# Performance work log

Hardware: AMD Instinct MI355X
Metric: run time of the kernel (lower is better)

The kernel has to match this reference:

```python
import jax, jax.numpy as jnp
import numpy as np

N_NODES = 50000
N_EDGES = 1600000
N_FEAT = 128
DROPOUT = 0.1


def setup_inputs() -> dict:
    key = jax.random.key(0)
    k1, k2, k3, k4 = jax.random.split(key, 4)
    x = jax.random.normal(k1, (N_NODES, N_FEAT), dtype=jnp.float32)
    adj_vals = jax.random.uniform(k2, (N_EDGES,), dtype=jnp.float32)
    row = jax.random.randint(k3, (N_EDGES,), 0, N_NODES, dtype=jnp.int32)
    col = jax.random.randint(k4, (N_EDGES,), 0, N_NODES, dtype=jnp.int32)
    return {"x": x, "adj_vals": adj_vals, "row": row, "col": col}


def reference(x, adj_vals, row, col):
    # MixedDropout on sparse adjacency values (deterministic fixed key),
    # then SpMM: out[i] = sum_{e: row[e]==i} A_drop[e] * x[col[e]]
    keep_prob = 1.0 - DROPOUT
    mask_key = jax.random.fold_in(jax.random.key(42), 7)
    keep = jax.random.bernoulli(mask_key, keep_prob, adj_vals.shape)
    vals_drop = jnp.where(keep, adj_vals / keep_prob, 0.0)
    # gather source features and weight by (dropped) edge values
    msgs = vals_drop[:, None] * x[col]  # [E, F]
    out = jax.ops.segment_sum(msgs, row, num_segments=N_NODES)  # [N, F]
    return out
```

## Files before the change

### kernel.cpp

```cpp
#include <hip/hip_runtime.h>
#include <stdint.h>

#define N_NODES 50000
#define N_EDGES 1600000
#define N_FEAT 128
#define CAP 64
#define OVF_CAP 65536

#define RSHIFT 8
#define BROWS 256
#define NB 196
#define NWG_A 250
#define A_THREADS 1024
#define CHUNKS_PW 1600
#define CAPW 56


struct KeyPair { uint32_t a, b; };

__host__ __device__ constexpr inline uint32_t rotl32(uint32_t x, int r) {
  return (x << r) | (x >> (32 - r));
}

__host__ __device__ constexpr inline KeyPair threefry2x32(uint32_t k0, uint32_t k1,
                                                          uint32_t x0, uint32_t x1) {
  const uint32_t ks0 = k0, ks1 = k1, ks2 = k0 ^ k1 ^ 0x1BD11BDAu;
  x0 += ks0;
  x1 += ks1;
  const int rotA[4] = {13, 15, 26, 6};
  const int rotB[4] = {17, 29, 16, 24};
  const uint32_t ks[3] = {ks0, ks1, ks2};
  for (int i = 0; i < 5; ++i) {
    const int* rot = (i & 1) ? rotB : rotA;
    for (int j = 0; j < 4; ++j) {
      x0 += x1;
      x1 = rotl32(x1, rot[j]);
      x1 ^= x0;
    }
    x0 += ks[(i + 1) % 3];
    x1 += ks[(i + 2) % 3] + (uint32_t)(i + 1);
  }
  return {x0, x1};
}

constexpr KeyPair MASK_KEY = threefry2x32(0u, 42u, 0u, 7u);

__device__ inline bool edge_keep(uint32_t e) {
  KeyPair r = threefry2x32(MASK_KEY.a, MASK_KEY.b, 0u, e);
  uint32_t bits = r.a ^ r.b;
  float u = __uint_as_float((bits >> 9) | 0x3f800000u) - 1.0f;
  return u < 0.9f;
}

__device__ inline uint32_t f2bf(uint32_t b) {
  return (b + 0x7fffu + ((b >> 16) & 1u)) >> 16;
}

typedef uint32_t u2v __attribute__((ext_vector_type(2)));
typedef float f4v __attribute__((ext_vector_type(4)));


__global__ void __launch_bounds__(A_THREADS) convA_kernel(const float* __restrict__ x,
                                                          uint32_t* __restrict__ xb,
                                                          const float* __restrict__ adj_vals,
                                                          const int* __restrict__ row,
                                                          const int* __restrict__ col,
                                                          uint64_t* __restrict__ coarse,
                                                          uint32_t* __restrict__ lens,
                                                          uint32_t* __restrict__ ovf_count,
                                                          uint64_t* __restrict__ ovf) {
  __shared__ uint32_t cnt[NB];
  int wg = blockIdx.x;
  int tid = threadIdx.x;
  if (tid < NB) cnt[tid] = 0;

  const int gthreads = NWG_A * A_THREADS;
  for (int i = wg * A_THREADS + tid; i < (N_NODES * N_FEAT) / 4; i += gthreads) {
    float4 f = ((const float4*)x)[i];
    u2v o;
    o.x = f2bf(__float_as_uint(f.x)) | (f2bf(__float_as_uint(f.y)) << 16);
    o.y = f2bf(__float_as_uint(f.z)) | (f2bf(__float_as_uint(f.w)) << 16);
    __builtin_nontemporal_store(o, (u2v*)xb + i);
  }
  __syncthreads();

  for (int ch = tid; ch < CHUNKS_PW; ch += A_THREADS) {
    const int g = wg * CHUNKS_PW + ch;
    const int4 r4 = ((const int4*)row)[g];
    const int4 c4 = ((const int4*)col)[g];
    const float4 a4 = ((const float4*)adj_vals)[g];
    const int rr[4] = {r4.x, r4.y, r4.z, r4.w};
    const int cc[4] = {c4.x, c4.y, c4.z, c4.w};
    const float aa[4] = {a4.x, a4.y, a4.z, a4.w};
#pragma unroll
    for (int k = 0; k < 4; ++k) {
      const uint32_t e = (uint32_t)(4 * g + k);
      if (!edge_keep(e)) continue;
      const uint32_t r = (uint32_t)rr[k];
      const uint32_t c = (uint32_t)cc[k];
      const float v = aa[k] / 0.9f;
      const uint32_t b = r >> RSHIFT;
      const uint32_t li = atomicAdd(&cnt[b], 1u);
      const uint64_t p = ((uint64_t)r << 48) | ((uint64_t)c << 32) | (uint64_t)__float_as_uint(v);
      if (li < CAPW) {
        __builtin_nontemporal_store(p, coarse + ((size_t)b * NWG_A + wg) * CAPW + li);
      } else {
        const uint32_t oi = atomicAdd(ovf_count, 1u);
        if (oi < OVF_CAP) ovf[oi] = p;
      }
    }
  }
  __syncthreads();
  if (tid < NB) lens[(size_t)tid * NWG_A + wg] = min(cnt[tid], (uint32_t)CAPW);
}

__global__ void __launch_bounds__(1024) partB_kernel(const uint64_t* __restrict__ coarse,
                                                     const uint32_t* __restrict__ lens,
                                                     uint32_t* __restrict__ payload,
                                                     uint32_t* __restrict__ cursor,
                                                     uint32_t* __restrict__ ovf_count,
                                                     uint64_t* __restrict__ ovf) {
  int b = blockIdx.x;
  int tid = threadIdx.x;
  __shared__ uint32_t cnt[BROWS];
  if (tid < BROWS) cnt[tid] = 0;
  __syncthreads();

  int wave = tid >> 6;
  int lane = tid & 63;
  for (int seg = wave; seg < NWG_A; seg += 16) {
    uint32_t len = lens[(size_t)b * NWG_A + seg];
    if (lane < (int)len) {
      uint64_t p = coarse[((size_t)b * NWG_A + seg) * CAPW + lane];
      uint32_t r = (uint32_t)(p >> 48);
      uint32_t rl = r & (BROWS - 1);
      uint32_t idx = atomicAdd(&cnt[rl], 1u);
      if (idx < CAP) {
        uint32_t c = (uint32_t)(p >> 32) & 0xFFFFu;
        payload[(size_t)r * CAP + idx] = (c << 16) | f2bf((uint32_t)p);
      } else {
        uint32_t oi = atomicAdd(ovf_count, 1u);
        if (oi < OVF_CAP) ovf[oi] = p;
      }
    }
  }
  __syncthreads();
  if (tid < BROWS) {
    uint32_t r = ((uint32_t)b << RSHIFT) + (uint32_t)tid;
    if (r < N_NODES) cursor[r] = min(cnt[tid], (uint32_t)CAP);
  }
}

__global__ void __launch_bounds__(256) gather_bf16_kernel(const uint32_t* __restrict__ xb,
                                                          const uint32_t* __restrict__ payload,
                                                          const uint32_t* __restrict__ cursor,
                                                          float* __restrict__ out) {
  int r = blockIdx.x * 16 + (threadIdx.x >> 4);
  int lane = threadIdx.x & 15;
  uint32_t base = (uint32_t)r * CAP;
  uint32_t cnt = cursor[r];
  if (cnt > CAP) cnt = CAP;
  const uint4* x4 = (const uint4*)xb;

  float acc0 = 0.f, acc1 = 0.f, acc2 = 0.f, acc3 = 0.f;
  float acc4 = 0.f, acc5 = 0.f, acc6 = 0.f, acc7 = 0.f;

  uint32_t p0 = __builtin_nontemporal_load(payload + base + lane);
  uint32_t p1 = (cnt > 16u) ? __builtin_nontemporal_load(payload + base + 16 + lane) : 0u;
  uint32_t p2 = (cnt > 32u) ? __builtin_nontemporal_load(payload + base + 32 + lane) : 0u;
  uint32_t p3 = (cnt > 48u) ? __builtin_nontemporal_load(payload + base + 48 + lane) : 0u;

#define GSTEP(ww)                                                            \
  {                                                                          \
    uint32_t cc = (ww) >> 16;                                                \
    float vv = __uint_as_float((ww) << 16);                                  \
    uint4 a = x4[(size_t)cc * 16 + lane];                                    \
    acc0 += vv * __uint_as_float(a.x << 16);                                 \
    acc1 += vv * __uint_as_float(a.x & 0xffff0000u);                         \
    acc2 += vv * __uint_as_float(a.y << 16);                                 \
    acc3 += vv * __uint_as_float(a.y & 0xffff0000u);                         \
    acc4 += vv * __uint_as_float(a.z << 16);                                 \
    acc5 += vv * __uint_as_float(a.z & 0xffff0000u);                         \
    acc6 += vv * __uint_as_float(a.w << 16);                                 \
    acc7 += vv * __uint_as_float(a.w & 0xffff0000u);                         \
  }

#define PCHUNK(preg, mm)                                                     \
  for (int j = 0; j < (mm); j += 8) {                                        \
    int lim = (mm) - j;                                                      \
    uint32_t w0 = __shfl((preg), j + 0, 16);                                 \
    uint32_t w1 = __shfl((preg), j + 1, 16);                                 \
    uint32_t w2 = __shfl((preg), j + 2, 16);                                 \
    uint32_t w3 = __shfl((preg), j + 3, 16);                                 \
    uint32_t w4 = __shfl((preg), j + 4, 16);                                 \
    uint32_t w5 = __shfl((preg), j + 5, 16);                                 \
    uint32_t w6 = __shfl((preg), j + 6, 16);                                 \
    uint32_t w7 = __shfl((preg), j + 7, 16);                                 \
    w1 = (1 < lim) ? w1 : 0u;                                                \
    w2 = (2 < lim) ? w2 : 0u;                                                \
    w3 = (3 < lim) ? w3 : 0u;                                                \
    w4 = (4 < lim) ? w4 : 0u;                                                \
    w5 = (5 < lim) ? w5 : 0u;                                                \
    w6 = (6 < lim) ? w6 : 0u;                                                \
    w7 = (7 < lim) ? w7 : 0u;                                                \
    GSTEP(w0) GSTEP(w1) GSTEP(w2) GSTEP(w3)                                  \
    GSTEP(w4) GSTEP(w5) GSTEP(w6) GSTEP(w7)                                  \
  }

  int rem = (int)cnt;
  if (rem > 0) {
    PCHUNK(p0, min(rem, 16));
    rem -= 16;
    if (rem > 0) {
      PCHUNK(p1, min(rem, 16));
      rem -= 16;
      if (rem > 0) {
        PCHUNK(p2, min(rem, 16));
        rem -= 16;
        if (rem > 0) {
          PCHUNK(p3, min(rem, 16));
        }
      }
    }
  }
#undef PCHUNK
#undef GSTEP

  f4v lo, hi;
  lo.x = acc0; lo.y = acc1; lo.z = acc2; lo.w = acc3;
  hi.x = acc4; hi.y = acc5; hi.z = acc6; hi.w = acc7;
  f4v* o = (f4v*)out + (size_t)r * 32 + lane * 2;
  __builtin_nontemporal_store(lo, o);
  __builtin_nontemporal_store(hi, o + 1);
}

__global__ void __launch_bounds__(256) ovf_pack_kernel(const float* __restrict__ x,
                                                       const uint32_t* __restrict__ ovf_count,
                                                       const uint64_t* __restrict__ ovf,
                                                       float* __restrict__ out) {
  uint32_t n = *ovf_count;
  if (n > OVF_CAP) n = OVF_CAP;
  int g = (int)((blockIdx.x * blockDim.x + threadIdx.x) >> 7);
  int f = threadIdx.x & 127;
  const int ngroups = (64 * 256) >> 7;
  for (uint32_t oi = g; oi < n; oi += ngroups) {
    uint64_t p = ovf[oi];
    uint32_t r = (uint32_t)(p >> 48);
    uint32_t c = (uint32_t)((p >> 32) & 0xFFFFu);
    float v = __uint_as_float((uint32_t)p);
    atomicAdd(&out[(size_t)r * N_FEAT + f], v * x[(size_t)c * N_FEAT + f]);
  }
}


__global__ void __launch_bounds__(256) scatter_fused_kernel(const float* __restrict__ x,
                                                            const float* __restrict__ adj_vals,
                                                            const int* __restrict__ row,
                                                            const int* __restrict__ col,
                                                            float* __restrict__ out) {
  long long t = (long long)blockIdx.x * blockDim.x + threadIdx.x;
  int e = (int)(t >> 6);
  int lane = (int)(t & 63);
  if (e >= N_EDGES) return;
  if (!edge_keep((uint32_t)e)) return;
  float v = adj_vals[e] / 0.9f;
  float2 xf = *(const float2*)(x + (long long)col[e] * N_FEAT + lane * 2);
  float* dst = out + (long long)row[e] * N_FEAT + lane * 2;
  atomicAdd(dst, v * xf.x);
  atomicAdd(dst + 1, v * xf.y);
}


extern "C" void kernel_launch(void* const* d_in, const int* in_sizes, int n_in,
                              void* d_out, int out_size, void* d_ws, size_t ws_size,
                              hipStream_t stream) {
  const float* x        = (const float*)d_in[0];
  const float* adj_vals = (const float*)d_in[1];
  const int*   row      = (const int*)d_in[2];
  const int*   col      = (const int*)d_in[3];
  float* out = (float*)d_out;

  size_t a_ovfc    = 0;
  size_t a_cursor  = 256;
  size_t a_lens    = (a_cursor + (size_t)N_NODES * 4 + 255) & ~255ull;
  size_t a_ovf     = (a_lens + (size_t)NB * NWG_A * 4 + 255) & ~255ull;
  size_t a_coarse  = (a_ovf + (size_t)OVF_CAP * 8 + 255) & ~255ull;
  size_t a_payload = (a_coarse + (size_t)NB * NWG_A * CAPW * 8 + 255) & ~255ull;
  size_t a_xb      = (a_payload + (size_t)N_NODES * CAP * 4 + 255) & ~255ull;
  size_t need      = a_xb + (size_t)N_NODES * N_FEAT * 2;

  if (ws_size >= need) {
    uint32_t* ovf_count = (uint32_t*)((char*)d_ws + a_ovfc);
    uint32_t* cursor    = (uint32_t*)((char*)d_ws + a_cursor);
    uint32_t* lens      = (uint32_t*)((char*)d_ws + a_lens);
    uint64_t* ovf       = (uint64_t*)((char*)d_ws + a_ovf);
    uint64_t* coarse    = (uint64_t*)((char*)d_ws + a_coarse);
    uint32_t* payload   = (uint32_t*)((char*)d_ws + a_payload);
    uint32_t* xb        = (uint32_t*)((char*)d_ws + a_xb);

    hipMemsetAsync(ovf_count, 0, 4, stream);
    convA_kernel<<<NWG_A, A_THREADS, 0, stream>>>(x, xb, adj_vals, row, col,
                                                  coarse, lens, ovf_count, ovf);
    partB_kernel<<<NB, 1024, 0, stream>>>(coarse, lens, payload, cursor, ovf_count, ovf);
    gather_bf16_kernel<<<N_NODES / 16, 256, 0, stream>>>(xb, payload, cursor, out);
    ovf_pack_kernel<<<64, 256, 0, stream>>>(x, ovf_count, ovf, out);
  } else {
    hipMemsetAsync(d_out, 0, (size_t)out_size * sizeof(float), stream);
    long long total_threads = (long long)N_EDGES * 64;
    scatter_fused_kernel<<<(int)((total_threads + 255) / 256), 256, 0, stream>>>(
        x, adj_vals, row, col, out);
  }
}
```

Before: 162.0 us.

## Replace global overflow counter with per-block overflow regions and drop memset

Overflow handling moves from one global atomic counter, which had to be cleared with a memset before each run, to per-workgroup overflow regions with LDS counters that each block writes out at its end. This removes the memset launch and the global atomics. The bf16 conversion now writes 16 bytes per store instead of 8, and the nontemporal stores become normal stores. partB zero-pads each row's payload up to a multiple of 8 so the gather can drop its per-step masking, and the gather loads payload chunks lazily. The overflow kernel now exits early when every region count is zero, at the cost of scanning all 446 counts in each of its 64 blocks.

Result: slower. 169.4 us (+4.5%).

```diff
diff --git a/kernel.cpp b/kernel.cpp
--- a/kernel.cpp
+++ b/kernel.cpp
@@ -5,7 +5,8 @@
 #define N_EDGES 1600000
 #define N_FEAT 128
 #define CAP 64
-#define OVF_CAP 65536
+#define OVF_PW 256
+#define OVF_PB 192
 
 #define RSHIFT 8
 #define BROWS 256
@@ -14,6 +15,7 @@
 #define A_THREADS 1024
 #define CHUNKS_PW 1600
 #define CAPW 56
+#define NREG (NWG_A + NB)
 
 
 struct KeyPair { uint32_t a, b; };
@@ -56,7 +58,7 @@
   return (b + 0x7fffu + ((b >> 16) & 1u)) >> 16;
 }
 
-typedef uint32_t u2v __attribute__((ext_vector_type(2)));
+typedef uint32_t u4v __attribute__((ext_vector_type(4)));
 typedef float f4v __attribute__((ext_vector_type(4)));
 
 
@@ -67,20 +69,25 @@
                                                           const int* __restrict__ col,
                                                           uint64_t* __restrict__ coarse,
                                                           uint32_t* __restrict__ lens,
-                                                          uint32_t* __restrict__ ovf_count,
-                                                          uint64_t* __restrict__ ovf) {
+                                                          uint32_t* __restrict__ ovfcA,
+                                                          uint64_t* __restrict__ ovfA) {
   __shared__ uint32_t cnt[NB];
+  __shared__ uint32_t ovfc;
   int wg = blockIdx.x;
   int tid = threadIdx.x;
   if (tid < NB) cnt[tid] = 0;
+  if (tid == 0) ovfc = 0;
 
   const int gthreads = NWG_A * A_THREADS;
-  for (int i = wg * A_THREADS + tid; i < (N_NODES * N_FEAT) / 4; i += gthreads) {
-    float4 f = ((const float4*)x)[i];
-    u2v o;
-    o.x = f2bf(__float_as_uint(f.x)) | (f2bf(__float_as_uint(f.y)) << 16);
-    o.y = f2bf(__float_as_uint(f.z)) | (f2bf(__float_as_uint(f.w)) << 16);
-    __builtin_nontemporal_store(o, (u2v*)xb + i);
+  for (int i = wg * A_THREADS + tid; i < (N_NODES * N_FEAT) / 8; i += gthreads) {
+    f4v a = ((const f4v*)x)[2 * i];
+    f4v b = ((const f4v*)x)[2 * i + 1];
+    u4v o;
+    o.x = f2bf(__float_as_uint(a.x)) | (f2bf(__float_as_uint(a.y)) << 16);
+    o.y = f2bf(__float_as_uint(a.z)) | (f2bf(__float_as_uint(a.w)) << 16);
+    o.z = f2bf(__float_as_uint(b.x)) | (f2bf(__float_as_uint(b.y)) << 16);
+    o.w = f2bf(__float_as_uint(b.z)) | (f2bf(__float_as_uint(b.w)) << 16);
+    ((u4v*)xb)[i] = o;
   }
   __syncthreads();
 
@@ -103,33 +110,38 @@
       const uint32_t li = atomicAdd(&cnt[b], 1u);
       const uint64_t p = ((uint64_t)r << 48) | ((uint64_t)c << 32) | (uint64_t)__float_as_uint(v);
       if (li < CAPW) {
-        __builtin_nontemporal_store(p, coarse + ((size_t)b * NWG_A + wg) * CAPW + li);
+        coarse[((size_t)b * NWG_A + wg) * CAPW + li] = p;
       } else {
-        const uint32_t oi = atomicAdd(ovf_count, 1u);
-        if (oi < OVF_CAP) ovf[oi] = p;
+        const uint32_t oi = atomicAdd(&ovfc, 1u);
+        if (oi < OVF_PW) ovfA[(size_t)wg * OVF_PW + oi] = p;
       }
     }
   }
   __syncthreads();
   if (tid < NB) lens[(size_t)tid * NWG_A + wg] = min(cnt[tid], (uint32_t)CAPW);
+  if (tid == 0) ovfcA[wg] = min(ovfc, (uint32_t)OVF_PW);
 }
 
 __global__ void __launch_bounds__(1024) partB_kernel(const uint64_t* __restrict__ coarse,
                                                      const uint32_t* __restrict__ lens,
                                                      uint32_t* __restrict__ payload,
                                                      uint32_t* __restrict__ cursor,
-                                                     uint32_t* __restrict__ ovf_count,
-                                                     uint64_t* __restrict__ ovf) {
+                                                     uint32_t* __restrict__ ovfcB,
+                                                     uint64_t* __restrict__ ovfB) {
   int b = blockIdx.x;
   int tid = threadIdx.x;
   __shared__ uint32_t cnt[BROWS];
+  __shared__ uint32_t s_len[NWG_A];
+  __shared__ uint32_t ovfc;
   if (tid < BROWS) cnt[tid] = 0;
+  if (tid < NWG_A) s_len[tid] = lens[(size_t)b * NWG_A + tid];
+  if (tid == 0) ovfc = 0;
   __syncthreads();
 
   int wave = tid >> 6;
   int lane = tid & 63;
   for (int seg = wave; seg < NWG_A; seg += 16) {
-    uint32_t len = lens[(size_t)b * NWG_A + seg];
+    uint32_t len = s_len[seg];
     if (lane < (int)len) {
       uint64_t p = coarse[((size_t)b * NWG_A + seg) * CAPW + lane];
       uint32_t r = (uint32_t)(p >> 48);
@@ -139,16 +151,22 @@
         uint32_t c = (uint32_t)(p >> 32) & 0xFFFFu;
         payload[(size_t)r * CAP + idx] = (c << 16) | f2bf((uint32_t)p);
       } else {
-        uint32_t oi = atomicAdd(ovf_count, 1u);
-        if (oi < OVF_CAP) ovf[oi] = p;
+        uint32_t oi = atomicAdd(&ovfc, 1u);
+        if (oi < OVF_PB) ovfB[(size_t)b * OVF_PB + oi] = p;
       }
     }
   }
   __syncthreads();
   if (tid < BROWS) {
     uint32_t r = ((uint32_t)b << RSHIFT) + (uint32_t)tid;
-    if (r < N_NODES) cursor[r] = min(cnt[tid], (uint32_t)CAP);
-  }
+    if (r < N_NODES) {
+      uint32_t c0 = min(cnt[tid], (uint32_t)CAP);
+      cursor[r] = c0;
+      uint32_t np = min((c0 + 7u) & ~7u, (uint32_t)CAP);
+      for (uint32_t i2 = c0; i2 < np; ++i2) payload[(size_t)r * CAP + i2] = 0u;
+    }
+  }
+  if (tid == 0) ovfcB[b] = min(ovfc, (uint32_t)OVF_PB);
 }
 
 __global__ void __launch_bounds__(256) gather_bf16_kernel(const uint32_t* __restrict__ xb,
@@ -159,16 +177,14 @@
   int lane = threadIdx.x & 15;
   uint32_t base = (uint32_t)r * CAP;
   uint32_t cnt = cursor[r];
-  if (cnt > CAP) cnt = CAP;
+  uint32_t n = (cnt + 7u) & ~7u;
   const uint4* x4 = (const uint4*)xb;
 
   float acc0 = 0.f, acc1 = 0.f, acc2 = 0.f, acc3 = 0.f;
   float acc4 = 0.f, acc5 = 0.f, acc6 = 0.f, acc7 = 0.f;
 
   uint32_t p0 = __builtin_nontemporal_load(payload + base + lane);
-  uint32_t p1 = (cnt > 16u) ? __builtin_nontemporal_load(payload + base + 16 + lane) : 0u;
-  uint32_t p2 = (cnt > 32u) ? __builtin_nontemporal_load(payload + base + 32 + lane) : 0u;
-  uint32_t p3 = (cnt > 48u) ? __builtin_nontemporal_load(payload + base + 48 + lane) : 0u;
+  uint32_t p1 = __builtin_nontemporal_load(payload + base + 16 + lane);
 
 #define GSTEP(ww)                                                            \
   {                                                                          \
@@ -187,7 +203,6 @@
 
 #define PCHUNK(preg, mm)                                                     \
   for (int j = 0; j < (mm); j += 8) {                                        \
-    int lim = (mm) - j;                                                      \
     uint32_t w0 = __shfl((preg), j + 0, 16);                                 \
     uint32_t w1 = __shfl((preg), j + 1, 16);                                 \
     uint32_t w2 = __shfl((preg), j + 2, 16);                                 \
@@ -196,30 +211,23 @@
     uint32_t w5 = __shfl((preg), j + 5, 16);                                 \
     uint32_t w6 = __shfl((preg), j + 6, 16);                                 \
     uint32_t w7 = __shfl((preg), j + 7, 16);                                 \
-    w1 = (1 < lim) ? w1 : 0u;                                                \
-    w2 = (2 < lim) ? w2 : 0u;                                                \
-    w3 = (3 < lim) ? w3 : 0u;                                                \
-    w4 = (4 < lim) ? w4 : 0u;                                                \
-    w5 = (5 < lim) ? w5 : 0u;                                                \
-    w6 = (6 < lim) ? w6 : 0u;                                                \
-    w7 = (7 < lim) ? w7 : 0u;                                                \
     GSTEP(w0) GSTEP(w1) GSTEP(w2) GSTEP(w3)                                  \
     GSTEP(w4) GSTEP(w5) GSTEP(w6) GSTEP(w7)                                  \
   }
 
-  int rem = (int)cnt;
+  int rem = (int)n;
+  PCHUNK(p0, min(rem, 16));
+  rem -= 16;
   if (rem > 0) {
-    PCHUNK(p0, min(rem, 16));
+    PCHUNK(p1, min(rem, 16));
     rem -= 16;
     if (rem > 0) {
-      PCHUNK(p1, min(rem, 16));
+      uint32_t p2 = __builtin_nontemporal_load(payload + base + 32 + lane);
+      PCHUNK(p2, min(rem, 16));
       rem -= 16;
       if (rem > 0) {
-        PCHUNK(p2, min(rem, 16));
-        rem -= 16;
-        if (rem > 0) {
-          PCHUNK(p3, min(rem, 16));
-        }
+        uint32_t p3 = __builtin_nontemporal_load(payload + base + 48 + lane);
+        PCHUNK(p3, min(rem, 16));
       }
     }
   }
@@ -235,20 +243,40 @@
 }
 
 __global__ void __launch_bounds__(256) ovf_pack_kernel(const float* __restrict__ x,
-                                                       const uint32_t* __restrict__ ovf_count,
-                                                       const uint64_t* __restrict__ ovf,
+                                                       const uint32_t* __restrict__ ovfcA,
+                                                       const uint64_t* __restrict__ ovfA,
+                                                       const uint32_t* __restrict__ ovfcB,
+                                                       const uint64_t* __restrict__ ovfB,
                                                        float* __restrict__ out) {
-  uint32_t n = *ovf_count;
-  if (n > OVF_CAP) n = OVF_CAP;
-  int g = (int)((blockIdx.x * blockDim.x + threadIdx.x) >> 7);
+  __shared__ int any;
+  if (threadIdx.x == 0) any = 0;
+  __syncthreads();
+  for (int t = threadIdx.x; t < NREG; t += 256) {
+    uint32_t c = (t < NWG_A) ? ovfcA[t] : ovfcB[t - NWG_A];
+    if (c) any = 1;
+  }
+  __syncthreads();
+  if (!any) return;
+
+  int group = (int)((blockIdx.x * 256 + threadIdx.x) >> 7);
   int f = threadIdx.x & 127;
-  const int ngroups = (64 * 256) >> 7;
-  for (uint32_t oi = g; oi < n; oi += ngroups) {
-    uint64_t p = ovf[oi];
-    uint32_t r = (uint32_t)(p >> 48);
-    uint32_t c = (uint32_t)((p >> 32) & 0xFFFFu);
-    float v = __uint_as_float((uint32_t)p);
-    atomicAdd(&out[(size_t)r * N_FEAT + f], v * x[(size_t)c * N_FEAT + f]);
+  for (int reg = group; reg < NREG; reg += 128) {
+    uint32_t c;
+    const uint64_t* basep;
+    if (reg < NWG_A) {
+      c = min(ovfcA[reg], (uint32_t)OVF_PW);
+      basep = ovfA + (size_t)reg * OVF_PW;
+    } else {
+      c = min(ovfcB[reg - NWG_A], (uint32_t)OVF_PB);
+      basep = ovfB + (size_t)(reg - NWG_A) * OVF_PB;
+    }
+    for (uint32_t i = 0; i < c; ++i) {
+      uint64_t p = basep[i];
+      uint32_t r = (uint32_t)(p >> 48);
+      uint32_t cc = (uint32_t)((p >> 32) & 0xFFFFu);
+      float v = __uint_as_float((uint32_t)p);
+      atomicAdd(&out[(size_t)r * N_FEAT + f], v * x[(size_t)cc * N_FEAT + f]);
+    }
   }
 }
 
@@ -280,30 +308,33 @@
   const int*   col      = (const int*)d_in[3];
   float* out = (float*)d_out;
 
-  size_t a_ovfc    = 0;
-  size_t a_cursor  = 256;
-  size_t a_lens    = (a_cursor + (size_t)N_NODES * 4 + 255) & ~255ull;
-  size_t a_ovf     = (a_lens + (size_t)NB * NWG_A * 4 + 255) & ~255ull;
-  size_t a_coarse  = (a_ovf + (size_t)OVF_CAP * 8 + 255) & ~255ull;
+  size_t a_cursor  = 0;
+  size_t a_ovfcA   = (a_cursor + (size_t)N_NODES * 4 + 255) & ~255ull;
+  size_t a_ovfcB   = (a_ovfcA + (size_t)NWG_A * 4 + 255) & ~255ull;
+  size_t a_lens    = (a_ovfcB + (size_t)NB * 4 + 255) & ~255ull;
+  size_t a_ovfA    = (a_lens + (size_t)NB * NWG_A * 4 + 255) & ~255ull;
+  size_t a_ovfB    = (a_ovfA + (size_t)NWG_A * OVF_PW * 8 + 255) & ~255ull;
+  size_t a_coarse  = (a_ovfB + (size_t)NB * OVF_PB * 8 + 255) & ~255ull;
   size_t a_payload = (a_coarse + (size_t)NB * NWG_A * CAPW * 8 + 255) & ~255ull;
   size_t a_xb      = (a_payload + (size_t)N_NODES * CAP * 4 + 255) & ~255ull;
   size_t need      = a_xb + (size_t)N_NODES * N_FEAT * 2;
 
   if (ws_size >= need) {
-    uint32_t* ovf_count = (uint32_t*)((char*)d_ws + a_ovfc);
-    uint32_t* cursor    = (uint32_t*)((char*)d_ws + a_cursor);
-    uint32_t* lens      = (uint32_t*)((char*)d_ws + a_lens);
-    uint64_t* ovf       = (uint64_t*)((char*)d_ws + a_ovf);
-    uint64_t* coarse    = (uint64_t*)((char*)d_ws + a_coarse);
-    uint32_t* payload   = (uint32_t*)((char*)d_ws + a_payload);
-    uint32_t* xb        = (uint32_t*)((char*)d_ws + a_xb);
-
-    hipMemsetAsync(ovf_count, 0, 4, stream);
+    uint32_t* cursor  = (uint32_t*)((char*)d_ws + a_cursor);
+    uint32_t* ovfcA   = (uint32_t*)((char*)d_ws + a_ovfcA);
+    uint32_t* ovfcB   = (uint32_t*)((char*)d_ws + a_ovfcB);
+    uint32_t* lens    = (uint32_t*)((char*)d_ws + a_lens);
+    uint64_t* ovfA    = (uint64_t*)((char*)d_ws + a_ovfA);
+    uint64_t* ovfB    = (uint64_t*)((char*)d_ws + a_ovfB);
+    uint64_t* coarse  = (uint64_t*)((char*)d_ws + a_coarse);
+    uint32_t* payload = (uint32_t*)((char*)d_ws + a_payload);
+    uint32_t* xb      = (uint32_t*)((char*)d_ws + a_xb);
+
     convA_kernel<<<NWG_A, A_THREADS, 0, stream>>>(x, xb, adj_vals, row, col,
-                                                  coarse, lens, ovf_count, ovf);
-    partB_kernel<<<NB, 1024, 0, stream>>>(coarse, lens, payload, cursor, ovf_count, ovf);
+                                                  coarse, lens, ovfcA, ovfA);
+    partB_kernel<<<NB, 1024, 0, stream>>>(coarse, lens, payload, cursor, ovfcB, ovfB);
     gather_bf16_kernel<<<N_NODES / 16, 256, 0, stream>>>(xb, payload, cursor, out);
-    ovf_pack_kernel<<<64, 256, 0, stream>>>(x, ovf_count, ovf, out);
+    ovf_pack_kernel<<<64, 256, 0, stream>>>(x, ovfcA, ovfA, ovfcB, ovfB, out);
   } else {
     hipMemsetAsync(d_out, 0, (size_t)out_size * sizeof(float), stream);
     long long total_threads = (long long)N_EDGES * 64;
```
